# Kernel tuning notes

Measured on AMD Instinct MI355X. Metric: run time of the kernel, lower is better.

The kernel has to match this reference:

```python
import jax, jax.numpy as jnp
import numpy as np

N, E, C, H, G = 100000, 1600000, 128, 64, 512
TOL = 1e-7          # PyG topk tolerance
MIN_SCORE = 0.05
EPS_KL = 1e-14


def setup_inputs() -> dict:
    key = jax.random.key(0)
    ks = jax.random.split(key, 12)
    d = {}
    d["x"] = jax.random.normal(ks[0], (N, C), jnp.float32)
    d["edge_index"] = jax.random.randint(ks[1], (2, E), 0, N)
    d["batch"] = jnp.sort(jax.random.randint(ks[2], (N,), 0, G))
    d["attn"] = jax.random.uniform(ks[3], (N,), jnp.float32, minval=1e-3, maxval=1.0)
    def lin(k, i, o):
        return (jax.random.normal(k, (i, o), jnp.float32) / np.sqrt(i)).astype(jnp.float32)
    d["W1"] = lin(ks[4], C, H); d["b1"] = jnp.zeros((H,), jnp.float32)
    d["W2"] = lin(ks[5], H, H); d["b2"] = jnp.zeros((H,), jnp.float32)
    d["pool_w"] = (jax.random.normal(ks[6], (C,), jnp.float32) / np.sqrt(C)).astype(jnp.float32)
    d["W3"] = lin(ks[7], H, H); d["b3"] = jnp.zeros((H,), jnp.float32)
    d["W4"] = lin(ks[8], H, H); d["b4"] = jnp.zeros((H,), jnp.float32)
    d["Wl"] = lin(ks[9], H, 1); d["bl"] = jnp.zeros((1,), jnp.float32)
    return d


def _gin(x, src, dst, Wa, ba, Wb, bb, edge_w=None):
    # GINConv with eps=0: nn((1+0)*x + sum_{j in N(i)} x_j), nn = Lin-ReLU-Lin
    msg = x[src]                                   # [E, F] gather
    if edge_w is not None:
        msg = msg * edge_w[:, None]                # drop pruned edges
    agg = jax.ops.segment_sum(msg, dst, num_segments=x.shape[0])
    h = x + agg
    return jax.nn.relu(h @ Wa + ba) @ Wb + bb


def reference(x, edge_index, batch, attn, W1, b1, W2, b2, pool_w, W3, b3, W4, b4, Wl, bl):
    src, dst = edge_index[0], edge_index[1]
    out = jax.nn.relu(_gin(x, src, dst, W1, b1, W2, b2))

    # --- TopKPooling(min_score=0.05), attn=x ---
    raw = x @ pool_w                               # [N] attention logits
    m = jax.ops.segment_max(raw, batch, num_segments=G)
    e = jnp.exp(raw - m[batch])
    z = jax.ops.segment_sum(e, batch, num_segments=G)
    score = e / z[batch]                           # per-graph softmax
    smax = jax.ops.segment_max(score, batch, num_segments=G)
    thresh = jnp.minimum(smax[batch] - TOL, MIN_SCORE)
    mask = score > thresh                          # kept nodes (>=1 per graph)
    maskf = mask.astype(x.dtype)
    out = out * (score * maskf)[:, None]           # x[perm] * score[perm]
    edge_keep = maskf[src] * maskf[dst]            # filter_adj: both endpoints kept

    out = jax.nn.relu(_gin(out, src, dst, W3, b3, W4, b4, edge_w=edge_keep)) * maskf[:, None]
    graph_out = jax.ops.segment_sum(out, batch, num_segments=G)  # global_add_pool
    pred = (graph_out @ Wl + bl).reshape(-1)       # [G]

    # attn_loss = scatter_mean(kl_div(log(score+eps), attn[perm]), batch)
    kl = attn * (jnp.log(attn) - jnp.log(score + EPS_KL))
    cnt = jax.ops.segment_sum(maskf, batch, num_segments=G)
    attn_loss = jax.ops.segment_sum(kl * maskf, batch, num_segments=G) / jnp.maximum(cnt, 1.0)

    ratio = maskf.sum() / x.shape[0]
    return pred, attn_loss, ratio
```

## Files before the change

### kernel.cpp

```cpp
#include <hip/hip_runtime.h>
#include <math.h>

#define N_NODES 100000
#define N_EDGES 1600000
#define C_IN    128
#define H_DIM   64
#define G_GRAPHS 512
#define MAXG    4096
#define ELCAP   65536
#define KPG     32

__device__ __forceinline__ int lbound(const int* __restrict__ b, int val) {
    int lo = 0, hi = N_NODES;
    while (lo < hi) {
        int mid = (lo + hi) >> 1;
        if (b[mid] < val) lo = mid + 1; else hi = mid;
    }
    return lo;
}

__global__ void kraw(const float* __restrict__ x, const float* __restrict__ pool_w,
                     float* __restrict__ sc) {
    const int lane = threadIdx.x & 63;
    const int l32  = lane & 31;
    const int half = lane >> 5;
    const float4 pwv = ((const float4*)pool_w)[l32];
    const int wid = blockIdx.x * (blockDim.x >> 6) + (threadIdx.x >> 6);
    const int nw  = gridDim.x * (blockDim.x >> 6);
    for (int r0 = wid * 2; r0 < N_NODES; r0 += nw * 2) {
        int row = r0 + half;
        float4 xv = ((const float4*)(x + (size_t)row * C_IN))[l32];
        float pr = xv.x * pwv.x + xv.y * pwv.y + xv.z * pwv.z + xv.w * pwv.w;
        #pragma unroll
        for (int m = 16; m > 0; m >>= 1) pr += __shfl_xor(pr, m, 64);
        if (l32 == 0) sc[row] = pr;
    }
}

__global__ void kA3(const int* __restrict__ batch, const float* __restrict__ attn,
                    float* __restrict__ sc, unsigned int* __restrict__ kept_bits,
                    int* __restrict__ klist, int* __restrict__ kcnt,
                    float* __restrict__ B, float* __restrict__ out) {
    __shared__ float buf[MAXG];
    __shared__ float red[256];
    __shared__ int   lst[KPG];
    __shared__ int   cntk;
    const int g = blockIdx.x;
    const int t = threadIdx.x;
    const int ns = lbound(batch, g);
    const int ne = lbound(batch, g + 1);
    const int cn = ne - ns;
    if (cn <= 0) {
        if (t == 0) { out[G_GRAPHS + g] = 0.f; kcnt[g] = 0; }
        return;
    }
    if (t == 0) cntk = 0;
    float lmax = -3.4e38f;
    for (int i = t; i < cn; i += 256) { float r = sc[ns + i]; buf[i] = r; lmax = fmaxf(lmax, r); }
    red[t] = lmax; __syncthreads();
    for (int o = 128; o > 0; o >>= 1) { if (t < o) red[t] = fmaxf(red[t], red[t + o]); __syncthreads(); }
    float m = red[0]; __syncthreads();
    float lsum = 0.f;
    for (int i = t; i < cn; i += 256) { float e = expf(buf[i] - m); buf[i] = e; lsum += e; }
    red[t] = lsum; __syncthreads();
    for (int o = 128; o > 0; o >>= 1) { if (t < o) red[t] += red[t + o]; __syncthreads(); }
    float z = red[0]; __syncthreads();
    float lsm = -3.4e38f;
    for (int i = t; i < cn; i += 256) { float s = buf[i] / z; buf[i] = s; lsm = fmaxf(lsm, s); }
    red[t] = lsm; __syncthreads();
    for (int o = 128; o > 0; o >>= 1) { if (t < o) red[t] = fmaxf(red[t], red[t + o]); __syncthreads(); }
    float smax = red[0];
    float thresh = fminf(smax - 1e-7f, 0.05f);
    __syncthreads();
    float klacc = 0.f;
    for (int i = t; i < cn; i += 256) {
        float s = buf[i];
        if (s > thresh) {
            int n = ns + i;
            int p = atomicAdd(&cntk, 1);
            if (p < KPG) lst[p] = i;
            sc[n] = s;
            float a = attn[n];
            klacc += a * (logf(a) - logf(s + 1e-14f));
        }
    }
    red[t] = klacc; __syncthreads();
    for (int o = 128; o > 0; o >>= 1) { if (t < o) red[t] += red[t + o]; __syncthreads(); }
    int kc = cntk;
    int kcc = kc < KPG ? kc : KPG;
    if (t == 0) {
        out[G_GRAPHS + g] = (kc > 0) ? red[0] / (float)kc : 0.f;
        kcnt[g] = kcc;
    }
    for (int i = t; i < kcc; i += 256) {
        int n = ns + lst[i];
        klist[g * KPG + i] = n;
        atomicOr(&kept_bits[n >> 5], 1u << (n & 31));
    }
    __syncthreads();
    for (int j = t; j < kcc * H_DIM; j += 256)
        B[(size_t)(ns + lst[j >> 6]) * H_DIM + (j & 63)] = 0.f;
}

__device__ __forceinline__ void emit(bool hit, int s, int d, int* __restrict__ list,
                                     int cap, int* __restrict__ count, int lane) {
    unsigned long long bal = __ballot(hit);
    if (bal == 0ull) return;
    int leader = __ffsll((long long)bal) - 1;
    int cnt = __popcll(bal);
    int base = 0;
    if (lane == leader) base = atomicAdd(count, cnt);
    base = __shfl(base, leader, 64);
    if (hit) {
        int p = base + __popcll(bal & ((1ull << lane) - 1ull));
        if (p < cap) { list[p] = s; list[cap + p] = d; }
    }
}

__global__ void k5f2(const int* __restrict__ ei, const unsigned int* __restrict__ bits,
                     const float* __restrict__ x, const float* __restrict__ W1,
                     float* __restrict__ B, int* __restrict__ elsd,
                     int* __restrict__ elcount) {
    __shared__ float W1s[C_IN * H_DIM];
    __shared__ int ls[1024], ld[1024];
    __shared__ int c1;
    const int t = threadIdx.x;
    const int lane = t & 63;
    if (t == 0) c1 = 0;
    int t4 = blockIdx.x * 256 + t;
    bool valid = t4 < (N_EDGES / 4);
    int4 s4 = make_int4(0, 0, 0, 0), d4 = make_int4(0, 0, 0, 0);
    if (valid) {
        s4 = ((const int4*)ei)[t4];
        d4 = ((const int4*)(ei + N_EDGES))[t4];
    }
    __syncthreads();
    int sv[4] = {s4.x, s4.y, s4.z, s4.w};
    int dv[4] = {d4.x, d4.y, d4.z, d4.w};
    bool bk[4];
    #pragma unroll
    for (int q = 0; q < 4; ++q) {
        int ss = sv[q], dd = dv[q];
        bool kd = valid && (((bits[dd >> 5] >> (dd & 31)) & 1u) != 0u);
        bk[q] = kd && (((bits[ss >> 5] >> (ss & 31)) & 1u) != 0u);
        if (kd) { int p = atomicAdd(&c1, 1); ls[p] = ss; ld[p] = dd; }
    }
    #pragma unroll
    for (int q = 0; q < 4; ++q) emit(bk[q], sv[q], dv[q], elsd, ELCAP, elcount, lane);
    __syncthreads();
    const int nloc = c1;
    if (nloc == 0) return;
    for (int i = t; i < C_IN * H_DIM; i += 256) W1s[i] = W1[i];
    __syncthreads();
    const int w = t >> 6;
    for (int idx = w; idx < nloc; idx += 4) {
        int s = ls[idx];
        int d = ld[idx];
        const float4* xr = (const float4*)(x + (size_t)s * C_IN);
        float acc = 0.f;
        #pragma unroll 8
        for (int k4 = 0; k4 < C_IN / 4; ++k4) {
            float4 xv = xr[k4];
            acc = fmaf(xv.x, W1s[(4 * k4 + 0) * H_DIM + lane], acc);
            acc = fmaf(xv.y, W1s[(4 * k4 + 1) * H_DIM + lane], acc);
            acc = fmaf(xv.z, W1s[(4 * k4 + 2) * H_DIM + lane], acc);
            acc = fmaf(xv.w, W1s[(4 * k4 + 3) * H_DIM + lane], acc);
        }
        atomicAdd(&B[(size_t)d * H_DIM + lane], acc);
    }
}

__global__ void k6w(const int* __restrict__ klist, const int* __restrict__ kcnt,
                    const float* __restrict__ sc, const float* __restrict__ x,
                    const float* __restrict__ W1,
                    const float* __restrict__ b1, const float* __restrict__ W2,
                    const float* __restrict__ b2, const float* __restrict__ W3,
                    float* __restrict__ A, float* __restrict__ B) {
    const int g = blockIdx.x;
    const int lane = threadIdx.x;
    const int kc = kcnt[g];
    const float b1l = b1[lane], b2l = b2[lane];
    for (int i = 0; i < kc; ++i) {
        int n = __builtin_amdgcn_readfirstlane(klist[g * KPG + i]);
        const float4* xr = (const float4*)(x + (size_t)n * C_IN);
        float u = 0.f;
        #pragma unroll 8
        for (int k4 = 0; k4 < C_IN / 4; ++k4) {
            float4 xv = xr[k4];
            u = fmaf(xv.x, W1[(4 * k4 + 0) * H_DIM + lane], u);
            u = fmaf(xv.y, W1[(4 * k4 + 1) * H_DIM + lane], u);
            u = fmaf(xv.z, W1[(4 * k4 + 2) * H_DIM + lane], u);
            u = fmaf(xv.w, W1[(4 * k4 + 3) * H_DIM + lane], u);
        }
        float t1 = fmaxf(u + B[(size_t)n * H_DIM + lane] + b1l, 0.f);
        B[(size_t)n * H_DIM + lane] = 0.f;
        float o1 = b2l;
        #pragma unroll 8
        for (int k = 0; k < H_DIM; ++k) o1 = fmaf(__shfl(t1, k, 64), W2[k * H_DIM + lane], o1);
        o1 = fmaxf(o1, 0.f);
        float v = 0.f;
        #pragma unroll 8
        for (int k = 0; k < H_DIM; ++k) v = fmaf(__shfl(o1, k, 64), W3[k * H_DIM + lane], v);
        A[(size_t)n * H_DIM + lane] = v * sc[n];
    }
}

__global__ void k7_scatter2(const int* __restrict__ elsd, const int* __restrict__ elcount,
                            const float* __restrict__ A, float* __restrict__ B) {
    const int lane = threadIdx.x & 63;
    const int wid  = blockIdx.x * (blockDim.x >> 6) + (threadIdx.x >> 6);
    const int nw   = gridDim.x * (blockDim.x >> 6);
    int ec = *elcount; if (ec > ELCAP) ec = ELCAP;
    for (int idx = wid; idx < ec; idx += nw) {
        int s = __builtin_amdgcn_readfirstlane(elsd[idx]);
        int d = __builtin_amdgcn_readfirstlane(elsd[ELCAP + idx]);
        atomicAdd(&B[(size_t)d * H_DIM + lane], A[(size_t)s * H_DIM + lane]);
    }
}

__global__ void k8b(const int* __restrict__ klist, const int* __restrict__ kcnt,
                    const float* __restrict__ b3, const float* __restrict__ W4,
                    const float* __restrict__ b4, const float* __restrict__ Wl,
                    const float* __restrict__ bl,
                    const float* __restrict__ A, const float* __restrict__ B,
                    float* __restrict__ out) {
    const int g = blockIdx.x;
    const int lane = threadIdx.x;
    const float b3l = b3[lane], b4l = b4[lane];
    const int kc = kcnt[g];
    float gsum = 0.f;
    for (int i = 0; i < kc; ++i) {
        int n = __builtin_amdgcn_readfirstlane(klist[g * KPG + i]);
        float t = fmaxf(A[(size_t)n * H_DIM + lane] + B[(size_t)n * H_DIM + lane] + b3l, 0.f);
        float o2 = b4l;
        #pragma unroll 8
        for (int k = 0; k < H_DIM; ++k) o2 = fmaf(__shfl(t, k, 64), W4[k * H_DIM + lane], o2);
        gsum += fmaxf(o2, 0.f);
    }
    float p = gsum * Wl[lane];
    #pragma unroll
    for (int m = 32; m > 0; m >>= 1) p += __shfl_xor(p, m, 64);
    if (lane == 0) out[g] = p + bl[0];
    if (g == 0) {
        int tot = 0;
        for (int i = lane; i < G_GRAPHS; i += 64) tot += kcnt[i];
        #pragma unroll
        for (int m = 32; m > 0; m >>= 1) tot += __shfl_xor(tot, m, 64);
        if (lane == 0) out[2 * G_GRAPHS] = (float)tot * (1.f / (float)N_NODES);
    }
}

extern "C" void kernel_launch(void* const* d_in, const int* in_sizes, int n_in,
                              void* d_out, int out_size, void* d_ws, size_t ws_size,
                              hipStream_t stream) {
    const float* x      = (const float*)d_in[0];
    const int*   ei     = (const int*)d_in[1];
    const int*   batch  = (const int*)d_in[2];
    const float* attn   = (const float*)d_in[3];
    const float* W1     = (const float*)d_in[4];
    const float* b1     = (const float*)d_in[5];
    const float* W2     = (const float*)d_in[6];
    const float* b2     = (const float*)d_in[7];
    const float* pool_w = (const float*)d_in[8];
    const float* W3     = (const float*)d_in[9];
    const float* b3     = (const float*)d_in[10];
    const float* W4     = (const float*)d_in[11];
    const float* b4     = (const float*)d_in[12];
    const float* Wl     = (const float*)d_in[13];
    const float* bl     = (const float*)d_in[14];
    float* out = (float*)d_out;

    float* A      = (float*)d_ws;
    float* B      = A + (size_t)N_NODES * H_DIM;
    float* sc     = B + (size_t)N_NODES * H_DIM;
    int*   klist  = (int*)(sc + N_NODES);
    int*   kcnt   = klist + G_GRAPHS * KPG;
    int*   elsd   = kcnt + G_GRAPHS;
    unsigned int* kept_bits = (unsigned int*)(elsd + 2 * ELCAP);
    int*          elcount   = (int*)(kept_bits + 3136);
    size_t zero_bytes = (size_t)((char*)(elcount + 1) - (char*)kept_bits);

    hipMemsetAsync(kept_bits, 0, zero_bytes, stream);

    kraw <<<2048, 256, 0, stream>>>(x, pool_w, sc);
    kA3  <<<G_GRAPHS, 256, 0, stream>>>(batch, attn, sc, kept_bits, klist, kcnt, B, out);
    k5f2 <<<(N_EDGES / 4 + 255) / 256, 256, 0, stream>>>(ei, kept_bits, x, W1, B,
                                                         elsd, elcount);
    k6w  <<<G_GRAPHS, 64, 0, stream>>>(klist, kcnt, sc, x, W1, b1, W2, b2, W3, A, B);
    k7_scatter2<<<32, 256, 0, stream>>>(elsd, elcount, A, B);
    k8b  <<<G_GRAPHS, 64, 0, stream>>>(klist, kcnt, b3, W4, b4, Wl, bl, A, B, out);
}
```

Measured before the change: 183.8 us.

## Fuse second GIN layer into one kernel and drop the memset and redundant reductions

The memset of the keep-bitmap and edge counter moves into the score kernel. That kernel now processes two rows per half-wave. The softmax block reductions use wavefront shuffles, and the separate score-max pass is replaced by 1/z, since the largest exponent is exactly 1. The k6w, k7_scatter2 and k8b kernels merge into one per-graph kernel. It scans the small kept-edge list for each kept node and recomputes each neighbour's first-layer output instead of storing it in A and scattering with atomics. This removes several launches and the A buffer, at the cost of redundant recompute and a linear edge scan per kept node.

```diff
diff --git a/kernel.cpp b/kernel.cpp
--- a/kernel.cpp
+++ b/kernel.cpp
@@ -9,6 +9,7 @@
 #define MAXG    4096
 #define ELCAP   65536
 #define KPG     32
+#define NBITS   3136
 
 __device__ __forceinline__ int lbound(const int* __restrict__ b, int val) {
     int lo = 0, hi = N_NODES;
@@ -19,34 +20,63 @@
     return lo;
 }
 
-__global__ void kraw(const float* __restrict__ x, const float* __restrict__ pool_w,
-                     float* __restrict__ sc) {
+__global__ void kpre(const float* __restrict__ x, const float* __restrict__ pool_w,
+                     float* __restrict__ sc, unsigned int* __restrict__ zero_region) {
+    int gid = blockIdx.x * blockDim.x + threadIdx.x;
+    if (gid < NBITS + 1) zero_region[gid] = 0u;
     const int lane = threadIdx.x & 63;
     const int l32  = lane & 31;
     const int half = lane >> 5;
     const float4 pwv = ((const float4*)pool_w)[l32];
     const int wid = blockIdx.x * (blockDim.x >> 6) + (threadIdx.x >> 6);
     const int nw  = gridDim.x * (blockDim.x >> 6);
-    for (int r0 = wid * 2; r0 < N_NODES; r0 += nw * 2) {
-        int row = r0 + half;
-        float4 xv = ((const float4*)(x + (size_t)row * C_IN))[l32];
-        float pr = xv.x * pwv.x + xv.y * pwv.y + xv.z * pwv.z + xv.w * pwv.w;
+    for (int r0 = wid * 4; r0 < N_NODES; r0 += nw * 4) {
+        int rowA = r0 + half;
+        int rowB = r0 + 2 + half;
+        float4 xa = ((const float4*)(x + (size_t)rowA * C_IN))[l32];
+        float4 xb = ((const float4*)(x + (size_t)rowB * C_IN))[l32];
+        float pa = xa.x * pwv.x + xa.y * pwv.y + xa.z * pwv.z + xa.w * pwv.w;
+        float pb = xb.x * pwv.x + xb.y * pwv.y + xb.z * pwv.z + xb.w * pwv.w;
         #pragma unroll
-        for (int m = 16; m > 0; m >>= 1) pr += __shfl_xor(pr, m, 64);
-        if (l32 == 0) sc[row] = pr;
-    }
-}
-
-__global__ void kA3(const int* __restrict__ batch, const float* __restrict__ attn,
+        for (int m = 16; m > 0; m >>= 1) {
+            pa += __shfl_xor(pa, m, 64);
+            pb += __shfl_xor(pb, m, 64);
+        }
+        if (l32 == 0) { sc[rowA] = pa; sc[rowB] = pb; }
+    }
+}
+
+__device__ __forceinline__ float blk_max(float v, float* red, int lane, int w) {
+    #pragma unroll
+    for (int m = 32; m > 0; m >>= 1) v = fmaxf(v, __shfl_xor(v, m, 64));
+    if (lane == 0) red[w] = v;
+    __syncthreads();
+    float r = fmaxf(fmaxf(red[0], red[1]), fmaxf(red[2], red[3]));
+    __syncthreads();
+    return r;
+}
+__device__ __forceinline__ float blk_sum(float v, float* red, int lane, int w) {
+    #pragma unroll
+    for (int m = 32; m > 0; m >>= 1) v += __shfl_xor(v, m, 64);
+    if (lane == 0) red[w] = v;
+    __syncthreads();
+    float r = (red[0] + red[1]) + (red[2] + red[3]);
+    __syncthreads();
+    return r;
+}
+
+__global__ void kA4(const int* __restrict__ batch, const float* __restrict__ attn,
                     float* __restrict__ sc, unsigned int* __restrict__ kept_bits,
                     int* __restrict__ klist, int* __restrict__ kcnt,
                     float* __restrict__ B, float* __restrict__ out) {
     __shared__ float buf[MAXG];
-    __shared__ float red[256];
+    __shared__ float red[4];
     __shared__ int   lst[KPG];
     __shared__ int   cntk;
     const int g = blockIdx.x;
     const int t = threadIdx.x;
+    const int lane = t & 63;
+    const int w = t >> 6;
     const int ns = lbound(batch, g);
     const int ne = lbound(batch, g + 1);
     const int cn = ne - ns;
@@ -57,24 +87,14 @@
     if (t == 0) cntk = 0;
     float lmax = -3.4e38f;
     for (int i = t; i < cn; i += 256) { float r = sc[ns + i]; buf[i] = r; lmax = fmaxf(lmax, r); }
-    red[t] = lmax; __syncthreads();
-    for (int o = 128; o > 0; o >>= 1) { if (t < o) red[t] = fmaxf(red[t], red[t + o]); __syncthreads(); }
-    float m = red[0]; __syncthreads();
+    float m = blk_max(lmax, red, lane, w);
     float lsum = 0.f;
     for (int i = t; i < cn; i += 256) { float e = expf(buf[i] - m); buf[i] = e; lsum += e; }
-    red[t] = lsum; __syncthreads();
-    for (int o = 128; o > 0; o >>= 1) { if (t < o) red[t] += red[t + o]; __syncthreads(); }
-    float z = red[0]; __syncthreads();
-    float lsm = -3.4e38f;
-    for (int i = t; i < cn; i += 256) { float s = buf[i] / z; buf[i] = s; lsm = fmaxf(lsm, s); }
-    red[t] = lsm; __syncthreads();
-    for (int o = 128; o > 0; o >>= 1) { if (t < o) red[t] = fmaxf(red[t], red[t + o]); __syncthreads(); }
-    float smax = red[0];
-    float thresh = fminf(smax - 1e-7f, 0.05f);
-    __syncthreads();
+    float z = blk_sum(lsum, red, lane, w);
+    float thresh = fminf(1.f / z - 1e-7f, 0.05f);
     float klacc = 0.f;
     for (int i = t; i < cn; i += 256) {
-        float s = buf[i];
+        float s = buf[i] / z;
         if (s > thresh) {
             int n = ns + i;
             int p = atomicAdd(&cntk, 1);
@@ -84,21 +104,19 @@
             klacc += a * (logf(a) - logf(s + 1e-14f));
         }
     }
-    red[t] = klacc; __syncthreads();
-    for (int o = 128; o > 0; o >>= 1) { if (t < o) red[t] += red[t + o]; __syncthreads(); }
-    int kc = cntk;
-    int kcc = kc < KPG ? kc : KPG;
+    float klsum = blk_sum(klacc, red, lane, w);
+    int kct = cntk;
+    int kc = kct < KPG ? kct : KPG;
     if (t == 0) {
-        out[G_GRAPHS + g] = (kc > 0) ? red[0] / (float)kc : 0.f;
-        kcnt[g] = kcc;
-    }
-    for (int i = t; i < kcc; i += 256) {
+        out[G_GRAPHS + g] = (kct > 0) ? klsum / (float)kct : 0.f;
+        kcnt[g] = kc;
+    }
+    for (int i = t; i < kc; i += 256) {
         int n = ns + lst[i];
         klist[g * KPG + i] = n;
         atomicOr(&kept_bits[n >> 5], 1u << (n & 31));
     }
-    __syncthreads();
-    for (int j = t; j < kcc * H_DIM; j += 256)
+    for (int j = t; j < kc * H_DIM; j += 256)
         B[(size_t)(ns + lst[j >> 6]) * H_DIM + (j & 63)] = 0.f;
 }
 
@@ -170,68 +188,67 @@
     }
 }
 
-__global__ void k6w(const int* __restrict__ klist, const int* __restrict__ kcnt,
+__device__ __forceinline__ float computeA(int n, int lane,
+                                          const float* __restrict__ x,
+                                          const float* __restrict__ B,
+                                          const float* __restrict__ sc,
+                                          const float* __restrict__ W1, float b1l,
+                                          const float* __restrict__ W2, float b2l,
+                                          const float* __restrict__ W3) {
+    const float4* xr = (const float4*)(x + (size_t)n * C_IN);
+    float u = 0.f;
+    #pragma unroll 8
+    for (int k4 = 0; k4 < C_IN / 4; ++k4) {
+        float4 xv = xr[k4];
+        u = fmaf(xv.x, W1[(4 * k4 + 0) * H_DIM + lane], u);
+        u = fmaf(xv.y, W1[(4 * k4 + 1) * H_DIM + lane], u);
+        u = fmaf(xv.z, W1[(4 * k4 + 2) * H_DIM + lane], u);
+        u = fmaf(xv.w, W1[(4 * k4 + 3) * H_DIM + lane], u);
+    }
+    float t1 = fmaxf(u + B[(size_t)n * H_DIM + lane] + b1l, 0.f);
+    float o1 = b2l;
+    #pragma unroll 8
+    for (int k = 0; k < H_DIM; ++k) o1 = fmaf(__shfl(t1, k, 64), W2[k * H_DIM + lane], o1);
+    o1 = fmaxf(o1, 0.f);
+    float v = 0.f;
+    #pragma unroll 8
+    for (int k = 0; k < H_DIM; ++k) v = fmaf(__shfl(o1, k, 64), W3[k * H_DIM + lane], v);
+    return v * sc[n];
+}
+
+__global__ void k8c(const int* __restrict__ klist, const int* __restrict__ kcnt,
                     const float* __restrict__ sc, const float* __restrict__ x,
-                    const float* __restrict__ W1,
-                    const float* __restrict__ b1, const float* __restrict__ W2,
-                    const float* __restrict__ b2, const float* __restrict__ W3,
-                    float* __restrict__ A, float* __restrict__ B) {
+                    const float* __restrict__ W1, const float* __restrict__ b1,
+                    const float* __restrict__ W2, const float* __restrict__ b2,
+                    const float* __restrict__ W3, const float* __restrict__ b3,
+                    const float* __restrict__ W4, const float* __restrict__ b4,
+                    const float* __restrict__ Wl, const float* __restrict__ bl,
+                    const float* __restrict__ B, const int* __restrict__ elsd,
+                    const int* __restrict__ elcount, float* __restrict__ out) {
     const int g = blockIdx.x;
     const int lane = threadIdx.x;
+    const float b1l = b1[lane], b2l = b2[lane], b3l = b3[lane], b4l = b4[lane];
     const int kc = kcnt[g];
-    const float b1l = b1[lane], b2l = b2[lane];
-    for (int i = 0; i < kc; ++i) {
-        int n = __builtin_amdgcn_readfirstlane(klist[g * KPG + i]);
-        const float4* xr = (const float4*)(x + (size_t)n * C_IN);
-        float u = 0.f;
-        #pragma unroll 8
-        for (int k4 = 0; k4 < C_IN / 4; ++k4) {
-            float4 xv = xr[k4];
-            u = fmaf(xv.x, W1[(4 * k4 + 0) * H_DIM + lane], u);
-            u = fmaf(xv.y, W1[(4 * k4 + 1) * H_DIM + lane], u);
-            u = fmaf(xv.z, W1[(4 * k4 + 2) * H_DIM + lane], u);
-            u = fmaf(xv.w, W1[(4 * k4 + 3) * H_DIM + lane], u);
-        }
-        float t1 = fmaxf(u + B[(size_t)n * H_DIM + lane] + b1l, 0.f);
-        B[(size_t)n * H_DIM + lane] = 0.f;
-        float o1 = b2l;
-        #pragma unroll 8
-        for (int k = 0; k < H_DIM; ++k) o1 = fmaf(__shfl(t1, k, 64), W2[k * H_DIM + lane], o1);
-        o1 = fmaxf(o1, 0.f);
-        float v = 0.f;
-        #pragma unroll 8
-        for (int k = 0; k < H_DIM; ++k) v = fmaf(__shfl(o1, k, 64), W3[k * H_DIM + lane], v);
-        A[(size_t)n * H_DIM + lane] = v * sc[n];
-    }
-}
-
-__global__ void k7_scatter2(const int* __restrict__ elsd, const int* __restrict__ elcount,
-                            const float* __restrict__ A, float* __restrict__ B) {
-    const int lane = threadIdx.x & 63;
-    const int wid  = blockIdx.x * (blockDim.x >> 6) + (threadIdx.x >> 6);
-    const int nw   = gridDim.x * (blockDim.x >> 6);
     int ec = *elcount; if (ec > ELCAP) ec = ELCAP;
-    for (int idx = wid; idx < ec; idx += nw) {
-        int s = __builtin_amdgcn_readfirstlane(elsd[idx]);
-        int d = __builtin_amdgcn_readfirstlane(elsd[ELCAP + idx]);
-        atomicAdd(&B[(size_t)d * H_DIM + lane], A[(size_t)s * H_DIM + lane]);
-    }
-}
-
-__global__ void k8b(const int* __restrict__ klist, const int* __restrict__ kcnt,
-                    const float* __restrict__ b3, const float* __restrict__ W4,
-                    const float* __restrict__ b4, const float* __restrict__ Wl,
-                    const float* __restrict__ bl,
-                    const float* __restrict__ A, const float* __restrict__ B,
-                    float* __restrict__ out) {
-    const int g = blockIdx.x;
-    const int lane = threadIdx.x;
-    const float b3l = b3[lane], b4l = b4[lane];
-    const int kc = kcnt[g];
     float gsum = 0.f;
     for (int i = 0; i < kc; ++i) {
         int n = __builtin_amdgcn_readfirstlane(klist[g * KPG + i]);
-        float t = fmaxf(A[(size_t)n * H_DIM + lane] + B[(size_t)n * H_DIM + lane] + b3l, 0.f);
+        float agg = 0.f;
+        for (int base = 0; base < ec; base += 64) {
+            int idx = base + lane;
+            int dd = (idx < ec) ? elsd[ELCAP + idx] : -1;
+            bool mtc = (dd == n);
+            int ssl = mtc ? elsd[idx] : 0;
+            unsigned long long bal = __ballot(mtc);
+            while (bal) {
+                int j = __ffsll((long long)bal) - 1;
+                bal &= bal - 1;
+                int s = __builtin_amdgcn_readfirstlane(__shfl(ssl, j, 64));
+                agg += computeA(s, lane, x, B, sc, W1, b1l, W2, b2l, W3);
+            }
+        }
+        float vA = computeA(n, lane, x, B, sc, W1, b1l, W2, b2l, W3);
+        float t = fmaxf(vA + agg + b3l, 0.f);
         float o2 = b4l;
         #pragma unroll 8
         for (int k = 0; k < H_DIM; ++k) o2 = fmaf(__shfl(t, k, 64), W4[k * H_DIM + lane], o2);
@@ -270,23 +287,18 @@
     const float* bl     = (const float*)d_in[14];
     float* out = (float*)d_out;
 
-    float* A      = (float*)d_ws;
-    float* B      = A + (size_t)N_NODES * H_DIM;
+    float* B      = (float*)d_ws;
     float* sc     = B + (size_t)N_NODES * H_DIM;
     int*   klist  = (int*)(sc + N_NODES);
     int*   kcnt   = klist + G_GRAPHS * KPG;
     int*   elsd   = kcnt + G_GRAPHS;
     unsigned int* kept_bits = (unsigned int*)(elsd + 2 * ELCAP);
-    int*          elcount   = (int*)(kept_bits + 3136);
-    size_t zero_bytes = (size_t)((char*)(elcount + 1) - (char*)kept_bits);
-
-    hipMemsetAsync(kept_bits, 0, zero_bytes, stream);
-
-    kraw <<<2048, 256, 0, stream>>>(x, pool_w, sc);
-    kA3  <<<G_GRAPHS, 256, 0, stream>>>(batch, attn, sc, kept_bits, klist, kcnt, B, out);
+    int*          elcount   = (int*)(kept_bits + NBITS);
+
+    kpre <<<2048, 256, 0, stream>>>(x, pool_w, sc, kept_bits);
+    kA4  <<<G_GRAPHS, 256, 0, stream>>>(batch, attn, sc, kept_bits, klist, kcnt, B, out);
     k5f2 <<<(N_EDGES / 4 + 255) / 256, 256, 0, stream>>>(ei, kept_bits, x, W1, B,
                                                          elsd, elcount);
-    k6w  <<<G_GRAPHS, 64, 0, stream>>>(klist, kcnt, sc, x, W1, b1, W2, b2, W3, A, B);
-    k7_scatter2<<<32, 256, 0, stream>>>(elsd, elcount, A, B);
-    k8b  <<<G_GRAPHS, 64, 0, stream>>>(klist, kcnt, b3, W4, b4, Wl, bl, A, B, out);
-}
+    k8c  <<<G_GRAPHS, 64, 0, stream>>>(klist, kcnt, sc, x, W1, b1, W2, b2, W3, b3,
+                                       W4, b4, Wl, bl, B, elsd, elcount, out);
+}
```

New measurement: 174.9 us. -4.8%, faster.
